# Performance work log

Measured on AMD Instinct MI355X. Metric: run time of the kernel, lower is better.

## Reference

```python
import jax, jax.numpy as jnp
import numpy as np

B, S, D, H, L = 2, 2048, 512, 8, 4
DK = D // H
FFN = 2048
CHUNK, LEFT, RIGHT = 64, 128, 32
EPS = 1e-3  # keras LayerNormalization default epsilon
NEG_INF = -1.0e9


def _banded_mask():
    # chunk-local emformer mask: row i in chunk c attends to [c*CHUNK-LEFT, (c+1)*CHUNK+RIGHT)
    m = np.zeros((S, S), np.int32)
    for c in range(S // CHUNK):
        r0, r1 = c * CHUNK, (c + 1) * CHUNK
        c0, c1 = max(0, r0 - LEFT), min(S, r1 + RIGHT)
        m[r0:r1, c0:c1] = 1
    return jnp.asarray(np.broadcast_to(m[None, None], (B, 1, S, S)))


def setup_inputs() -> dict:
    key = jax.random.key(0)
    ks = jax.random.split(key, 8)
    sd = 1.0 / np.sqrt(D)
    inp = {
        "x": jax.random.normal(ks[0], (B, S, D), jnp.float32),
        "mask": _banded_mask(),
        "Wq": jax.random.normal(ks[1], (L, D, D), jnp.float32) * sd,
        "bq": jnp.zeros((L, D), jnp.float32),
        "Wk": jax.random.normal(ks[2], (L, D, D), jnp.float32) * sd,
        "bk": jnp.zeros((L, D), jnp.float32),
        "Wv": jax.random.normal(ks[3], (L, D, D), jnp.float32) * sd,
        "bv": jnp.zeros((L, D), jnp.float32),
        "W1": jax.random.normal(ks[4], (L, D, FFN), jnp.float32) * sd,
        "b1": jnp.zeros((L, FFN), jnp.float32),
        "W2": jax.random.normal(ks[5], (L, FFN, D), jnp.float32) / np.sqrt(FFN),
        "b2": jnp.zeros((L, D), jnp.float32),
        "ln_in_g": jnp.ones((L, D), jnp.float32),
        "ln_in_b": jnp.zeros((L, D), jnp.float32),
        "ln1_g": jnp.ones((L, D), jnp.float32),
        "ln1_b": jnp.zeros((L, D), jnp.float32),
        "ln2_g": jnp.ones((L, D), jnp.float32),
        "ln2_b": jnp.zeros((L, D), jnp.float32),
    }
    return inp


def _ln(x, g, b):
    mu = jnp.mean(x, axis=-1, keepdims=True)
    var = jnp.mean(jnp.square(x - mu), axis=-1, keepdims=True)
    return (x - mu) * jax.lax.rsqrt(var + EPS) * g + b


def _block(x, maskf, Wq, bq, Wk, bk, Wv, bv, W1, b1, W2, b2, g_in, b_in, g1, bb1, g2, bb2):
    bs = x.shape[0]
    xl = _ln(x, g_in, b_in)
    q = (xl @ Wq + bq).reshape(bs, -1, H, DK).transpose(0, 2, 1, 3)  # [B,H,S,dk]
    k = (xl @ Wk + bk).reshape(bs, -1, H, DK).transpose(0, 2, 1, 3)
    v = (xl @ Wv + bv).reshape(bs, -1, H, DK).transpose(0, 2, 1, 3)
    scores = jnp.einsum("bhsd,bhtd->bhst", q, k) / np.sqrt(DK)
    scores = scores + NEG_INF * (1.0 - maskf)
    probs = jax.nn.softmax(scores, axis=-1)
    out = jnp.einsum("bhst,bhtd->bhsd", probs, v)
    out = out.transpose(0, 2, 1, 3).reshape(bs, -1, H * DK)
    out = out + x  # residual to block input (pre-LN)
    attn_out = _ln(out, g1, bb1)
    ffn = jax.nn.relu(attn_out @ W1 + b1) @ W2 + b2
    return _ln(ffn + attn_out, g2, bb2)


def reference(x, mask, Wq, bq, Wk, bk, Wv, bv, W1, b1, W2, b2,
              ln_in_g, ln_in_b, ln1_g, ln1_b, ln2_g, ln2_b):
    maskf = mask.astype(x.dtype)
    for i in range(L):
        x = _block(x, maskf, Wq[i], bq[i], Wk[i], bk[i], Wv[i], bv[i],
                   W1[i], b1[i], W2[i], b2[i],
                   ln_in_g[i], ln_in_b[i], ln1_g[i], ln1_b[i], ln2_g[i], ln2_b[i])
    return x
```

## Files before the change

kernel.cpp:

```cpp
#include <hip/hip_runtime.h>
#include <stdint.h>

#define DEVI __device__ __forceinline__

typedef __attribute__((ext_vector_type(8))) short bf16x8;
typedef __attribute__((ext_vector_type(4))) float f32x4;

DEVI short tobf(float v){
  uint32_t u = __builtin_bit_cast(uint32_t, v);
  uint32_t r = (u + 0x7fffu + ((u >> 16) & 1u)) >> 16;
  return (short)(uint16_t)r;
}

DEVI float frombf(short s){
  uint32_t u = ((uint32_t)(uint16_t)s) << 16;
  return __builtin_bit_cast(float, u);
}

DEVI f32x4 mfma16(bf16x8 a, bf16x8 b, f32x4 c){
  return __builtin_amdgcn_mfma_f32_16x16x32_bf16(a, b, c, 0, 0, 0);
}

DEVI void async16(const void* g, void* lds_uniform){
  __builtin_amdgcn_global_load_lds(
      (const __attribute__((address_space(1))) unsigned int*)g,
      (__attribute__((address_space(3))) unsigned int*)lds_uniform,
      16, 0, 0);
}

DEVI void ln_row_compute(const float* __restrict__ in, const float* __restrict__ in2,
                         const float* __restrict__ resf, const short* __restrict__ resb,
                         const float* __restrict__ cb,
                         const float* __restrict__ g, const float* __restrict__ be,
                         const float* __restrict__ gn, const float* __restrict__ bn,
                         float* __restrict__ outf, short* __restrict__ outb, int row)
{
  const int lane = threadIdx.x & 63;
  const size_t base = (size_t)row * 512 + lane * 8;
  const int col = lane * 8;
  f32x4 x0 = *(const f32x4*)(in + base);
  f32x4 x1 = *(const f32x4*)(in + base + 4);
  if (in2){
    f32x4 a0 = *(const f32x4*)(in2 + base), a1 = *(const f32x4*)(in2 + base + 4);
    x0 += a0; x1 += a1;
  }
  if (cb){
    f32x4 c0 = *(const f32x4*)(cb + col), c1 = *(const f32x4*)(cb + col + 4);
    x0 += c0; x1 += c1;
  }
  if (resf){
    f32x4 r0v = *(const f32x4*)(resf + base), r1v = *(const f32x4*)(resf + base + 4);
    x0 += r0v; x1 += r1v;
  }
  if (resb){
    bf16x8 rb = *(const bf16x8*)(resb + base);
    #pragma unroll
    for (int i = 0; i < 4; i++){ x0[i] += frombf(rb[i]); x1[i] += frombf(rb[i+4]); }
  }
  float s = x0[0]+x0[1]+x0[2]+x0[3]+x1[0]+x1[1]+x1[2]+x1[3];
  #pragma unroll
  for (int m = 1; m < 64; m <<= 1) s += __shfl_xor(s, m, 64);
  const float mu = s * (1.f/512.f);
  float vs = 0.f;
  #pragma unroll
  for (int i = 0; i < 4; i++){
    float d0 = x0[i]-mu; vs += d0*d0;
    float d1 = x1[i]-mu; vs += d1*d1;
  }
  #pragma unroll
  for (int m = 1; m < 64; m <<= 1) vs += __shfl_xor(vs, m, 64);
  const float rs = rsqrtf(vs * (1.f/512.f) + 1e-3f);
  f32x4 gv0 = *(const f32x4*)(g+col),  gv1 = *(const f32x4*)(g+col+4);
  f32x4 bv0 = *(const f32x4*)(be+col), bv1 = *(const f32x4*)(be+col+4);
  f32x4 y0, y1;
  #pragma unroll
  for (int i = 0; i < 4; i++){
    y0[i] = (x0[i]-mu)*rs*gv0[i] + bv0[i];
    y1[i] = (x1[i]-mu)*rs*gv1[i] + bv1[i];
  }
  if (outf){ *(f32x4*)(outf+base) = y0; *(f32x4*)(outf+base+4) = y1; }
  if (outb){
    f32x4 z0 = y0, z1 = y1;
    if (gn){
      float s2 = z0[0]+z0[1]+z0[2]+z0[3]+z1[0]+z1[1]+z1[2]+z1[3];
      #pragma unroll
      for (int m = 1; m < 64; m <<= 1) s2 += __shfl_xor(s2, m, 64);
      const float mu2 = s2 * (1.f/512.f);
      float v2 = 0.f;
      #pragma unroll
      for (int i = 0; i < 4; i++){
        float d0 = z0[i]-mu2; v2 += d0*d0;
        float d1 = z1[i]-mu2; v2 += d1*d1;
      }
      #pragma unroll
      for (int m = 1; m < 64; m <<= 1) v2 += __shfl_xor(v2, m, 64);
      const float rs2 = rsqrtf(v2 * (1.f/512.f) + 1e-3f);
      f32x4 gn0 = *(const f32x4*)(gn+col), gn1 = *(const f32x4*)(gn+col+4);
      f32x4 bn0 = *(const f32x4*)(bn+col), bn1 = *(const f32x4*)(bn+col+4);
      #pragma unroll
      for (int i = 0; i < 4; i++){
        z0[i] = (z0[i]-mu2)*rs2*gn0[i] + bn0[i];
        z1[i] = (z1[i]-mu2)*rs2*gn1[i] + bn1[i];
      }
    }
    bf16x8 ob;
    #pragma unroll
    for (int i = 0; i < 4; i++){ ob[i] = tobf(z0[i]); ob[i+4] = tobf(z1[i]); }
    *(bf16x8*)(outb + base) = ob;
  }
}

__global__ __launch_bounds__(256)
void transpose_all(const float* __restrict__ Wq, const float* __restrict__ Wk,
                   const float* __restrict__ Wv, const float* __restrict__ W1,
                   const float* __restrict__ W2,
                   short* __restrict__ WqkvT, short* __restrict__ W1T,
                   short* __restrict__ W2T,
                   const float* __restrict__ x_in, const float* __restrict__ gin,
                   const float* __restrict__ bin, short* __restrict__ xl)
{
  if (blockIdx.x >= 11264){
    const int row = ((blockIdx.x - 11264) << 2) + (threadIdx.x >> 6);
    ln_row_compute(x_in, nullptr, nullptr, nullptr, nullptr, gin, bin,
                   nullptr, nullptr, nullptr, xl, row);
    return;
  }
  __shared__ float tsh[32][33];
  const int l = blockIdx.x / 2816;
  const int t = blockIdx.x % 2816;
  const float* src; short* dst; int K, N, local;
  if (t < 768){
    const int m = t >> 8;
    src = (m==0 ? Wq : (m==1 ? Wk : Wv)) + (size_t)l*262144;
    dst = WqkvT + (size_t)l*786432 + m*262144; K = 512; N = 512; local = t & 255;
  } else if (t < 1792){
    src = W1 + (size_t)l*1048576; dst = W1T + (size_t)l*1048576;
    K = 512; N = 2048; local = t - 768;
  } else {
    src = W2 + (size_t)l*1048576; dst = W2T + (size_t)l*1048576;
    K = 2048; N = 512; local = t - 1792;
  }
  const int tnx = N >> 5;
  const int tc = (local % tnx) << 5, tr = (local / tnx) << 5;
  const int lr = threadIdx.x >> 5, lc = threadIdx.x & 31;
  #pragma unroll
  for (int i = 0; i < 32; i += 8)
    tsh[lr + i][lc] = src[(size_t)(tr + lr + i) * N + tc + lc];
  __syncthreads();
  #pragma unroll
  for (int i = 0; i < 32; i += 8)
    dst[(size_t)(tc + lr + i) * K + tr + lc] = tobf(tsh[lc][lr + i]);
}

__global__ __launch_bounds__(256)
void ln_kernel(const float* __restrict__ in, const float* __restrict__ in2,
               const float* __restrict__ resf, const short* __restrict__ resb,
               const float* __restrict__ cb,
               const float* __restrict__ g, const float* __restrict__ be,
               const float* __restrict__ gn, const float* __restrict__ bn,
               float* __restrict__ outf, short* __restrict__ outb)
{
  const int row = (blockIdx.x << 2) + (threadIdx.x >> 6);
  ln_row_compute(in, in2, resf, resb, cb, g, be, gn, bn, outf, outb, row);
}

template<int MODE, int BJ>
__global__ __launch_bounds__(256)
void gemm_bt(const short* __restrict__ A, const short* __restrict__ BT,
             int N, int K, int Ks,
             const float* __restrict__ b0, const float* __restrict__ b1p,
             const float* __restrict__ b2p, void* __restrict__ out0)
{
  constexpr int NTILE = 32*BJ;
  __shared__ __align__(16) short Ash[64*64];
  __shared__ __align__(16) short Bsh[NTILE*64];
  const int tid = threadIdx.x;
  const int wid = tid >> 6, lane = tid & 63;
  const int l15 = lane & 15, g4 = lane >> 4;
  const int nbn = N / NTILE;
  const int cpx = gridDim.x >> 3;
  int bid = blockIdx.x;
  bid = (bid & 7) * cpx + (bid >> 3);
  const int bm = bid / nbn, bn = bid % nbn;
  const int m0 = bm << 6, n0 = bn * NTILE;
  const int kofs = blockIdx.z * Ks;

  const short* aP[2]; const short* bP[BJ];
  #pragma unroll
  for (int p = 0; p < 2; p++){
    int u = p*256 + tid, row = u >> 3, sl = (u & 7) ^ (row & 7);
    aP[p] = A + (size_t)(m0 + row) * K + kofs + sl * 8;
  }
  #pragma unroll
  for (int p = 0; p < BJ; p++){
    int u = p*256 + tid, row = u >> 3, sl = (u & 7) ^ (row & 7);
    bP[p] = BT + (size_t)(n0 + row) * K + kofs + sl * 8;
  }
  char* ldsA = (char*)Ash;
  char* ldsB = (char*)Bsh;

  f32x4 acc[2][BJ] = {};
  const int wr = wid & 1, wc = wid >> 1;
  const int nkt = Ks >> 6;

  for (int kt = 0; kt < nkt; ++kt){
    const int k0 = kt << 6;
    #pragma unroll
    for (int p = 0; p < 2; p++)
      async16(aP[p] + k0, ldsA + (p*256 + wid*64) * 16);
    #pragma unroll
    for (int p = 0; p < BJ; p++)
      async16(bP[p] + k0, ldsB + (p*256 + wid*64) * 16);
    __syncthreads();
    #pragma unroll
    for (int ks = 0; ks < 2; ++ks){
      bf16x8 af[2], bfm[BJ];
      #pragma unroll
      for (int i = 0; i < 2; i++){
        const int ar = wr*32 + i*16 + l15;
        af[i] = *(const bf16x8*)&ldsA[ar*128 + (((ks<<2)+g4) ^ (ar&7))*16];
      }
      #pragma unroll
      for (int j = 0; j < BJ; j++){
        const int br = wc*(16*BJ) + j*16 + l15;
        bfm[j] = *(const bf16x8*)&ldsB[br*128 + (((ks<<2)+g4) ^ (br&7))*16];
      }
      #pragma unroll
      for (int i = 0; i < 2; i++)
        #pragma unroll
        for (int j = 0; j < BJ; j++)
          acc[i][j] = mfma16(af[i], bfm[j], acc[i][j]);
    }
    __syncthreads();
  }

  const int r0 = m0 + wr*32 + g4*4;
  const int cc0 = n0 + wc*(16*BJ) + l15;
  #pragma unroll
  for (int j = 0; j < BJ; j++){
    const int gc = cc0 + j*16;
    if (MODE == 0){
      const float bi = gc < 512 ? b0[gc] : (gc < 1024 ? b1p[gc-512] : b2p[gc-1024]);
      short* ob = (short*)out0;
      #pragma unroll
      for (int i = 0; i < 2; i++)
        #pragma unroll
        for (int r = 0; r < 4; r++){
          const int grow = r0 + i*16 + r;
          ob[(size_t)grow * N + gc] = tobf(acc[i][j][r] + bi);
        }
    } else if (MODE == 1){
      const float bi = b0[gc];
      short* ob = (short*)out0;
      #pragma unroll
      for (int i = 0; i < 2; i++)
        #pragma unroll
        for (int r = 0; r < 4; r++){
          const int grow = r0 + i*16 + r;
          float v = acc[i][j][r] + bi;
          v = fmaxf(v, 0.f);
          ob[(size_t)grow * N + gc] = tobf(v);
        }
    } else {
      float* ob = (float*)out0 + (size_t)blockIdx.z * 2097152;
      #pragma unroll
      for (int i = 0; i < 2; i++)
        #pragma unroll
        for (int r = 0; r < 4; r++){
          const int grow = r0 + i*16 + r;
          ob[(size_t)grow * N + gc] = acc[i][j][r];
        }
    }
  }
}

__global__ __launch_bounds__(256)
void attn_kernel(const short* __restrict__ qkv, float* __restrict__ attnO,
                 const float* __restrict__ resid)
{
  constexpr int NT = 14, NK2 = 7, VS = 232, LDQ = 1536;
  __shared__ __align__(16) short Vt[64*VS];
  __shared__ __align__(16) short Pl[4][16*VS];
  const int c = blockIdx.x, h = blockIdx.y, b = blockIdx.z;
  const int kb0 = 64*c - 128;
  const size_t rowbase = (size_t)b*2048;
  const short* Q     = qkv + (rowbase + 64*c)*LDQ + h*64;
  const short* Kbase = qkv + rowbase*LDQ + 512  + h*64;
  const short* Vbase = qkv + rowbase*LDQ + 1024 + h*64;
  const int tid = threadIdx.x, wid = tid >> 6, lane = tid & 63;
  const int l15 = lane & 15, g4 = lane >> 4;

  for (int idx = tid; idx < NT*16*64; idx += 256){
    const int t = idx >> 10, r = (idx >> 6) & 15, d = idx & 63;
    const int kb = kb0 + t*16;
    short v = 0;
    if (kb >= 0 && kb + 16 <= 2048) v = Vbase[(size_t)(kb + r)*LDQ + d];
    Vt[d*VS + t*16 + r] = v;
  }

  const short* qr = Q + (wid*16 + l15)*LDQ + g4*8;
  const bf16x8 aq0 = *(const bf16x8*)qr;
  const bf16x8 aq1 = *(const bf16x8*)(qr + 32);

  f32x4 sf[NT];
  #pragma unroll
  for (int t = 0; t < NT; t++){
    const int kb = kb0 + t*16;
    if (kb >= 0 && kb + 16 <= 2048){
      const short* kr = Kbase + (size_t)(kb + l15)*LDQ + g4*8;
      const bf16x8 k0 = *(const bf16x8*)kr;
      const bf16x8 k1 = *(const bf16x8*)(kr + 32);
      f32x4 z = {0.f,0.f,0.f,0.f};
      z = mfma16(aq0, k0, z);
      z = mfma16(aq1, k1, z);
      sf[t] = z;
    } else {
      sf[t] = (f32x4){-1e9f,-1e9f,-1e9f,-1e9f};
    }
  }

  float mx[4] = {-1e30f,-1e30f,-1e30f,-1e30f};
  #pragma unroll
  for (int t = 0; t < NT; t++)
    #pragma unroll
    for (int r = 0; r < 4; r++) mx[r] = fmaxf(mx[r], sf[t][r]);
  #pragma unroll
  for (int m = 1; m < 16; m <<= 1)
    #pragma unroll
    for (int r = 0; r < 4; r++) mx[r] = fmaxf(mx[r], __shfl_xor(mx[r], m, 64));

  float sum[4] = {0.f,0.f,0.f,0.f};
  #pragma unroll
  for (int t = 0; t < NT; t++)
    #pragma unroll
    for (int r = 0; r < 4; r++){
      const float p = __expf((sf[t][r] - mx[r]) * 0.125f);
      sf[t][r] = p; sum[r] += p;
    }
  #pragma unroll
  for (int m = 1; m < 16; m <<= 1)
    #pragma unroll
    for (int r = 0; r < 4; r++) sum[r] += __shfl_xor(sum[r], m, 64);
  float inv[4];
  #pragma unroll
  for (int r = 0; r < 4; r++) inv[r] = 1.f / sum[r];

  short* Pw = Pl[wid];
  #pragma unroll
  for (int t = 0; t < NT; t++)
    #pragma unroll
    for (int r = 0; r < 4; r++)
      Pw[(g4*4 + r)*VS + t*16 + l15] = tobf(sf[t][r]);

  __syncthreads();

  f32x4 ao[4] = {};
  #pragma unroll
  for (int ks = 0; ks < NK2; ks++){
    const bf16x8 pa = *(const bf16x8*)&Pw[l15*VS + ks*32 + g4*8];
    #pragma unroll
    for (int ni = 0; ni < 4; ni++){
      const bf16x8 vb = *(const bf16x8*)&Vt[(ni*16 + l15)*VS + ks*32 + g4*8];
      ao[ni] = mfma16(pa, vb, ao[ni]);
    }
  }

  const int orow = 64*c + wid*16 + g4*4;
  const size_t obase = ((size_t)b*2048 + orow)*512 + h*64;
  float* ob = attnO + obase;
  const float* rb = resid + obase;
  #pragma unroll
  for (int ni = 0; ni < 4; ni++)
    #pragma unroll
    for (int r = 0; r < 4; r++)
      ob[(size_t)r*512 + ni*16 + l15] = ao[ni][r] * inv[r] + rb[(size_t)r*512 + ni*16 + l15];
}

extern "C" void kernel_launch(void* const* d_in, const int* in_sizes, int n_in,
                              void* d_out, int out_size, void* d_ws, size_t ws_size,
                              hipStream_t stream)
{
  const float* x_in = (const float*)d_in[0];
  const float* Wq = (const float*)d_in[2];
  const float* bq = (const float*)d_in[3];
  const float* Wk = (const float*)d_in[4];
  const float* bk = (const float*)d_in[5];
  const float* Wv = (const float*)d_in[6];
  const float* bv = (const float*)d_in[7];
  const float* W1 = (const float*)d_in[8];
  const float* b1 = (const float*)d_in[9];
  const float* W2 = (const float*)d_in[10];
  const float* b2 = (const float*)d_in[11];
  const float* gin = (const float*)d_in[12];
  const float* bin = (const float*)d_in[13];
  const float* g1  = (const float*)d_in[14];
  const float* be1 = (const float*)d_in[15];
  const float* g2  = (const float*)d_in[16];
  const float* be2 = (const float*)d_in[17];

  char* ws = (char*)d_ws;
  size_t o = 0;
  float* xbuf  = (float*)(ws + o); o += (size_t)4096*512*4;
  short* xl    = (short*)(ws + o); o += (size_t)4096*512*2;
  short* qkv   = (short*)(ws + o); o += (size_t)4096*1536*2;
  float* attnO = (float*)(ws + o); o += (size_t)4096*512*4;
  short* h1    = (short*)(ws + o); o += (size_t)4096*2048*2;
  float* pbuf  = (float*)(ws + o); o += (size_t)2*4096*512*4;
  short* WqkvT = (short*)(ws + o); o += (size_t)4*1536*512*2;
  short* W1T   = (short*)(ws + o); o += (size_t)4*2048*512*2;
  short* W2T   = (short*)(ws + o); o += (size_t)4*512*2048*2;

  transpose_all<<<12288,256,0,stream>>>(Wq, Wk, Wv, W1, W2, WqkvT, W1T, W2T,
                                        x_in, gin, bin, xl);

  const float* xcur = x_in;
  for (int l = 0; l < 4; l++){
    gemm_bt<0,3><<<1024,256,0,stream>>>(xl, WqkvT + (size_t)l*786432, 1536, 512, 512,
                                        bq + l*512, bk + l*512, bv + l*512, qkv);
    attn_kernel<<<dim3(32,8,2),256,0,stream>>>(qkv, attnO, xcur);
    ln_kernel<<<1024,256,0,stream>>>(attnO, nullptr, nullptr, nullptr, nullptr,
                                     g1 + l*512, be1 + l*512, nullptr, nullptr,
                                     nullptr, xl);
    gemm_bt<1,4><<<1024,256,0,stream>>>(xl, W1T + (size_t)l*1048576, 2048, 512, 512,
                                        b1 + l*2048, nullptr, nullptr, h1);
    gemm_bt<3,2><<<dim3(512,1,2),256,0,stream>>>(h1, W2T + (size_t)l*1048576, 512, 2048, 1024,
                                                 nullptr, nullptr, nullptr, pbuf);
    if (l < 3){
      ln_kernel<<<1024,256,0,stream>>>(pbuf, pbuf + 2097152, nullptr, xl, b2 + l*512,
                                       g2 + l*512, be2 + l*512,
                                       gin + (l+1)*512, bin + (l+1)*512,
                                       xbuf, xl);
      xcur = xbuf;
    } else {
      ln_kernel<<<1024,256,0,stream>>>(pbuf, pbuf + 2097152, nullptr, xl, b2 + l*512,
                                       g2 + l*512, be2 + l*512,
                                       nullptr, nullptr, (float*)d_out, nullptr);
    }
  }
}
```

Measured before the change: 350.4 us.

## Load GEMM fragments directly from global memory, bypassing LDS staging

Removes the shared-memory tiles, async global-to-LDS copies and the two barriers per K-step from the bf16 GEMM. Each wave now reads its MFMA A and B fragments straight from global memory in 32-wide K steps, with the loop unrolled by 8 so loads can overlap. This drops the LDS round trip and synchronisation, but A and B data that waves used to share through LDS are now fetched redundantly by several waves, relying on L1/L2 to absorb the repeats.

```diff
diff --git a/kernel.cpp b/kernel.cpp
--- a/kernel.cpp
+++ b/kernel.cpp
@@ -19,13 +19,6 @@
 
 DEVI f32x4 mfma16(bf16x8 a, bf16x8 b, f32x4 c){
   return __builtin_amdgcn_mfma_f32_16x16x32_bf16(a, b, c, 0, 0, 0);
-}
-
-DEVI void async16(const void* g, void* lds_uniform){
-  __builtin_amdgcn_global_load_lds(
-      (const __attribute__((address_space(1))) unsigned int*)g,
-      (__attribute__((address_space(3))) unsigned int*)lds_uniform,
-      16, 0, 0);
 }
 
 DEVI void ln_row_compute(const float* __restrict__ in, const float* __restrict__ in2,
@@ -172,8 +165,6 @@
              const float* __restrict__ b2p, void* __restrict__ out0)
 {
   constexpr int NTILE = 32*BJ;
-  __shared__ __align__(16) short Ash[64*64];
-  __shared__ __align__(16) short Bsh[NTILE*64];
   const int tid = threadIdx.x;
   const int wid = tid >> 6, lane = tid & 63;
   const int l15 = lane & 15, g4 = lane >> 4;
@@ -184,58 +175,36 @@
   const int bm = bid / nbn, bn = bid % nbn;
   const int m0 = bm << 6, n0 = bn * NTILE;
   const int kofs = blockIdx.z * Ks;
-
-  const short* aP[2]; const short* bP[BJ];
-  #pragma unroll
-  for (int p = 0; p < 2; p++){
-    int u = p*256 + tid, row = u >> 3, sl = (u & 7) ^ (row & 7);
-    aP[p] = A + (size_t)(m0 + row) * K + kofs + sl * 8;
-  }
-  #pragma unroll
-  for (int p = 0; p < BJ; p++){
-    int u = p*256 + tid, row = u >> 3, sl = (u & 7) ^ (row & 7);
-    bP[p] = BT + (size_t)(n0 + row) * K + kofs + sl * 8;
-  }
-  char* ldsA = (char*)Ash;
-  char* ldsB = (char*)Bsh;
+  const int wr = wid & 1, wc = wid >> 1;
+
+  const short* ap[2]; const short* bp[BJ];
+  #pragma unroll
+  for (int i = 0; i < 2; i++)
+    ap[i] = A + (size_t)(m0 + wr*32 + i*16 + l15) * K + kofs + g4*8;
+  #pragma unroll
+  for (int j = 0; j < BJ; j++)
+    bp[j] = BT + (size_t)(n0 + wc*16*BJ + j*16 + l15) * K + kofs + g4*8;
 
   f32x4 acc[2][BJ] = {};
-  const int wr = wid & 1, wc = wid >> 1;
-  const int nkt = Ks >> 6;
-
+  const int nkt = Ks >> 5;
+
+  #pragma unroll 8
   for (int kt = 0; kt < nkt; ++kt){
-    const int k0 = kt << 6;
-    #pragma unroll
-    for (int p = 0; p < 2; p++)
-      async16(aP[p] + k0, ldsA + (p*256 + wid*64) * 16);
-    #pragma unroll
-    for (int p = 0; p < BJ; p++)
-      async16(bP[p] + k0, ldsB + (p*256 + wid*64) * 16);
-    __syncthreads();
-    #pragma unroll
-    for (int ks = 0; ks < 2; ++ks){
-      bf16x8 af[2], bfm[BJ];
-      #pragma unroll
-      for (int i = 0; i < 2; i++){
-        const int ar = wr*32 + i*16 + l15;
-        af[i] = *(const bf16x8*)&ldsA[ar*128 + (((ks<<2)+g4) ^ (ar&7))*16];
-      }
-      #pragma unroll
-      for (int j = 0; j < BJ; j++){
-        const int br = wc*(16*BJ) + j*16 + l15;
-        bfm[j] = *(const bf16x8*)&ldsB[br*128 + (((ks<<2)+g4) ^ (br&7))*16];
-      }
-      #pragma unroll
-      for (int i = 0; i < 2; i++)
-        #pragma unroll
-        for (int j = 0; j < BJ; j++)
-          acc[i][j] = mfma16(af[i], bfm[j], acc[i][j]);
-    }
-    __syncthreads();
+    const int ko = kt << 5;
+    bf16x8 af[2], bf[BJ];
+    #pragma unroll
+    for (int i = 0; i < 2; i++)  af[i] = *(const bf16x8*)(ap[i] + ko);
+    #pragma unroll
+    for (int j = 0; j < BJ; j++) bf[j] = *(const bf16x8*)(bp[j] + ko);
+    #pragma unroll
+    for (int i = 0; i < 2; i++)
+      #pragma unroll
+      for (int j = 0; j < BJ; j++)
+        acc[i][j] = mfma16(af[i], bf[j], acc[i][j]);
   }
 
   const int r0 = m0 + wr*32 + g4*4;
-  const int cc0 = n0 + wc*(16*BJ) + l15;
+  const int cc0 = n0 + wc*16*BJ + l15;
   #pragma unroll
   for (int j = 0; j < BJ; j++){
     const int gc = cc0 + j*16;
```

Result: slower. 765.4 us (+118.4%).

## Parametrize GEMM K-tile, drop split-K for W2, vectorize V transpose load

Applied to the files above, without the earlier changes.

Adds a BK template parameter so the QKV and W2 GEMMs use 128-wide K tiles, halving the number of barrier-separated iterations. The W2 GEMM no longer splits K across two z-slices: it writes a single fp32 output with the bias fused in, so the following layernorm reads one buffer instead of summing two partials. The attention kernel's V transpose now loads 8 bf16 values per thread with a vector load instead of scalar loads. The trade-off is larger LDS tiles and only 512 blocks for the W2 GEMM, which lowers occupancy and parallelism in exchange for less partial-sum traffic.

```diff
diff --git a/kernel.cpp b/kernel.cpp
--- a/kernel.cpp
+++ b/kernel.cpp
@@ -164,16 +164,19 @@
   ln_row_compute(in, in2, resf, resb, cb, g, be, gn, bn, outf, outb, row);
 }
 
-template<int MODE, int BJ>
+template<int MODE, int BJ, int BK>
 __global__ __launch_bounds__(256)
 void gemm_bt(const short* __restrict__ A, const short* __restrict__ BT,
-             int N, int K, int Ks,
+             int N, int K,
              const float* __restrict__ b0, const float* __restrict__ b1p,
              const float* __restrict__ b2p, void* __restrict__ out0)
 {
   constexpr int NTILE = 32*BJ;
-  __shared__ __align__(16) short Ash[64*64];
-  __shared__ __align__(16) short Bsh[NTILE*64];
+  constexpr int UPR = BK/8;
+  constexpr int AU = 64*UPR/256;
+  constexpr int BU = NTILE*UPR/256;
+  __shared__ __align__(16) short Ash[64*BK];
+  __shared__ __align__(16) short Bsh[NTILE*BK];
   const int tid = threadIdx.x;
   const int wid = tid >> 6, lane = tid & 63;
   const int l15 = lane & 15, g4 = lane >> 4;
@@ -183,47 +186,46 @@
   bid = (bid & 7) * cpx + (bid >> 3);
   const int bm = bid / nbn, bn = bid % nbn;
   const int m0 = bm << 6, n0 = bn * NTILE;
-  const int kofs = blockIdx.z * Ks;
-
-  const short* aP[2]; const short* bP[BJ];
-  #pragma unroll
-  for (int p = 0; p < 2; p++){
-    int u = p*256 + tid, row = u >> 3, sl = (u & 7) ^ (row & 7);
-    aP[p] = A + (size_t)(m0 + row) * K + kofs + sl * 8;
-  }
-  #pragma unroll
-  for (int p = 0; p < BJ; p++){
-    int u = p*256 + tid, row = u >> 3, sl = (u & 7) ^ (row & 7);
-    bP[p] = BT + (size_t)(n0 + row) * K + kofs + sl * 8;
+
+  const short* aP[AU]; const short* bP[BU];
+  #pragma unroll
+  for (int p = 0; p < AU; p++){
+    int u = p*256 + tid, row = u / UPR, sl = (u % UPR) ^ (row & (UPR-1));
+    aP[p] = A + (size_t)(m0 + row) * K + sl * 8;
+  }
+  #pragma unroll
+  for (int p = 0; p < BU; p++){
+    int u = p*256 + tid, row = u / UPR, sl = (u % UPR) ^ (row & (UPR-1));
+    bP[p] = BT + (size_t)(n0 + row) * K + sl * 8;
   }
   char* ldsA = (char*)Ash;
   char* ldsB = (char*)Bsh;
 
   f32x4 acc[2][BJ] = {};
   const int wr = wid & 1, wc = wid >> 1;
-  const int nkt = Ks >> 6;
+  const int nkt = K / BK;
 
   for (int kt = 0; kt < nkt; ++kt){
-    const int k0 = kt << 6;
-    #pragma unroll
-    for (int p = 0; p < 2; p++)
+    const int k0 = kt * BK;
+    #pragma unroll
+    for (int p = 0; p < AU; p++)
       async16(aP[p] + k0, ldsA + (p*256 + wid*64) * 16);
     #pragma unroll
-    for (int p = 0; p < BJ; p++)
+    for (int p = 0; p < BU; p++)
       async16(bP[p] + k0, ldsB + (p*256 + wid*64) * 16);
     __syncthreads();
     #pragma unroll
-    for (int ks = 0; ks < 2; ++ks){
+    for (int ks = 0; ks < BK/32; ++ks){
       bf16x8 af[2], bfm[BJ];
       #pragma unroll
       for (int i = 0; i < 2; i++){
         const int ar = wr*32 + i*16 + l15;
-        af[i] = *(const bf16x8*)&ldsA[ar*128 + (((ks<<2)+g4) ^ (ar&7))*16];
+        af[i] = *(const bf16x8*)&ldsA[ar*(2*BK) + (((ks<<2)+g4) ^ (ar&(UPR-1)))*16];
       }
       #pragma unroll
       for (int j = 0; j < BJ; j++){
         const int br = wc*(16*BJ) + j*16 + l15;
-        bfm[j] = *(const bf16x8*)&ldsB[br*128 + (((ks<<2)+g4) ^ (br&7))*16];
+        bfm[j] = *(const bf16x8*)&ldsB[br*(2*BK) + (((ks<<2)+g4) ^ (br&(UPR-1)))*16];
       }
       #pragma unroll
       for (int i = 0; i < 2; i++)
@@ -235,7 +237,7 @@
   }
 
   const int r0 = m0 + wr*32 + g4*4;
-  const int cc0 = n0 + wc*(16*BJ) + l15;
+  const int cc0 = n0 + wc*16*BJ + l15;
   #pragma unroll
   for (int j = 0; j < BJ; j++){
     const int gc = cc0 + j*16;
@@ -262,13 +264,14 @@
           ob[(size_t)grow * N + gc] = tobf(v);
         }
     } else {
-      float* ob = (float*)out0 + (size_t)blockIdx.z * 2097152;
+      const float bi = b0[gc];
+      float* ob = (float*)out0;
       #pragma unroll
       for (int i = 0; i < 2; i++)
         #pragma unroll
         for (int r = 0; r < 4; r++){
           const int grow = r0 + i*16 + r;
-          ob[(size_t)grow * N + gc] = acc[i][j][r];
+          ob[(size_t)grow * N + gc] = acc[i][j][r] + bi;
         }
     }
   }
@@ -290,12 +293,16 @@
   const int tid = threadIdx.x, wid = tid >> 6, lane = tid & 63;
   const int l15 = lane & 15, g4 = lane >> 4;
 
-  for (int idx = tid; idx < NT*16*64; idx += 256){
-    const int t = idx >> 10, r = (idx >> 6) & 15, d = idx & 63;
+  for (int idx = tid; idx < NT*16*8; idx += 256){
+    const int t = idx >> 7, rem = idx & 127;
+    const int r = rem >> 3, d8 = (rem & 7) << 3;
     const int kb = kb0 + t*16;
-    short v = 0;
-    if (kb >= 0 && kb + 16 <= 2048) v = Vbase[(size_t)(kb + r)*LDQ + d];
-    Vt[d*VS + t*16 + r] = v;
+    bf16x8 v = {0,0,0,0,0,0,0,0};
+    if (kb >= 0 && kb + 16 <= 2048)
+      v = *(const bf16x8*)(Vbase + (size_t)(kb + r)*LDQ + d8);
+    short* dst = &Vt[d8*VS + t*16 + r];
+    #pragma unroll
+    for (int e = 0; e < 8; e++) dst[e*VS] = v[e];
   }
 
   const short* qr = Q + (wid*16 + l15)*LDQ + g4*8;
@@ -405,7 +412,7 @@
   short* qkv   = (short*)(ws + o); o += (size_t)4096*1536*2;
   float* attnO = (float*)(ws + o); o += (size_t)4096*512*4;
   short* h1    = (short*)(ws + o); o += (size_t)4096*2048*2;
-  float* pbuf  = (float*)(ws + o); o += (size_t)2*4096*512*4;
+  float* pbuf  = (float*)(ws + o); o += (size_t)4096*512*4;
   short* WqkvT = (short*)(ws + o); o += (size_t)4*1536*512*2;
   short* W1T   = (short*)(ws + o); o += (size_t)4*2048*512*2;
   short* W2T   = (short*)(ws + o); o += (size_t)4*512*2048*2;
@@ -415,24 +422,24 @@
 
   const float* xcur = x_in;
   for (int l = 0; l < 4; l++){
-    gemm_bt<0,3><<<1024,256,0,stream>>>(xl, WqkvT + (size_t)l*786432, 1536, 512, 512,
-                                        bq + l*512, bk + l*512, bv + l*512, qkv);
+    gemm_bt<0,3,128><<<1024,256,0,stream>>>(xl, WqkvT + (size_t)l*786432, 1536, 512,
+                                            bq + l*512, bk + l*512, bv + l*512, qkv);
     attn_kernel<<<dim3(32,8,2),256,0,stream>>>(qkv, attnO, xcur);
     ln_kernel<<<1024,256,0,stream>>>(attnO, nullptr, nullptr, nullptr, nullptr,
                                      g1 + l*512, be1 + l*512, nullptr, nullptr,
                                      nullptr, xl);
-    gemm_bt<1,4><<<1024,256,0,stream>>>(xl, W1T + (size_t)l*1048576, 2048, 512, 512,
-                                        b1 + l*2048, nullptr, nullptr, h1);
-    gemm_bt<3,2><<<dim3(512,1,2),256,0,stream>>>(h1, W2T + (size_t)l*1048576, 512, 2048, 1024,
-                                                 nullptr, nullptr, nullptr, pbuf);
+    gemm_bt<1,4,64><<<1024,256,0,stream>>>(xl, W1T + (size_t)l*1048576, 2048, 512,
+                                           b1 + l*2048, nullptr, nullptr, h1);
+    gemm_bt<3,2,128><<<512,256,0,stream>>>(h1, W2T + (size_t)l*1048576, 512, 2048,
+                                           b2 + l*512, nullptr, nullptr, pbuf);
     if (l < 3){
-      ln_kernel<<<1024,256,0,stream>>>(pbuf, pbuf + 2097152, nullptr, xl, b2 + l*512,
+      ln_kernel<<<1024,256,0,stream>>>(pbuf, nullptr, nullptr, xl, nullptr,
                                        g2 + l*512, be2 + l*512,
                                        gin + (l+1)*512, bin + (l+1)*512,
                                        xbuf, xl);
       xcur = xbuf;
     } else {
-      ln_kernel<<<1024,256,0,stream>>>(pbuf, pbuf + 2097152, nullptr, xl, b2 + l*512,
+      ln_kernel<<<1024,256,0,stream>>>(pbuf, nullptr, nullptr, xl, nullptr,
                                        g2 + l*512, be2 + l*512,
                                        nullptr, nullptr, (float*)d_out, nullptr);
     }
```

New measurement: 297.9 us. 1.18x faster.
